# Optimization experiments

Hardware: AMD Instinct MI355X
Metric: run time of the kernel (lower is better)

The kernel has to match this reference:

```python
import jax, jax.numpy as jnp
import numpy as np

B, D, H, W, K = 32, 128, 128, 128, 32

def setup_inputs() -> dict:
    key = jax.random.key(0)
    k1, k2, k3 = jax.random.split(key, 3)
    X = jax.random.normal(k1, (B, D, H, W), dtype=jnp.float32)
    std1 = 1.0 / np.sqrt(K * D)
    codewords = jax.random.uniform(k2, (K, D), dtype=jnp.float32, minval=-std1, maxval=std1)
    scale = jax.random.uniform(k3, (K,), dtype=jnp.float32, minval=-1.0, maxval=0.0)
    return {"X": X, "codewords": codewords, "scale": scale}

def reference(X, codewords, scale):
    # X: [B, D, H, W] -> [B, N, D]
    b, d = X.shape[0], X.shape[1]
    x = X.reshape(b, d, -1).transpose(0, 2, 1)  # [B, N, D]
    x2 = jnp.sum(x * x, axis=-1, keepdims=True)            # [B, N, 1]
    c2 = jnp.sum(codewords * codewords, axis=-1)           # [K]
    xc = jnp.einsum('bnd,kd->bnk', x, codewords)           # [B, N, K]
    sl = scale * (x2 - 2.0 * xc + c2)                      # [B, N, K]
    A = jax.nn.softmax(sl, axis=2)                         # assignment weights
    # E[b,k,d] = sum_n A[b,n,k] * (x[b,n,d] - c[k,d])
    E = jnp.einsum('bnk,bnd->bkd', A, x) - jnp.sum(A, axis=1)[..., None] * codewords
    return E
```

## Files before the change

kernel.cpp:

```cpp
#include <hip/hip_runtime.h>

#define B_      32
#define D_      128
#define N_      16384
#define K_      32
#define NCHUNK  16
#define CSZ     (N_ / NCHUNK)
#define NS      512
#define NSUB    (CSZ / NS)
#define AST_STRIDE 520

#define WS_CT    0
#define WS_SC    4096
#define WS_SM2   4128
#define WS_C2S   4160
#define WS_ASUMP 4352
#define WS_EP    24576

typedef __attribute__((ext_vector_type(8))) short bf16x8;
typedef __attribute__((ext_vector_type(4))) float f32x4;

static __device__ inline unsigned short f2bf(float f) {
    unsigned int u = __float_as_uint(f);
    u += 0x7fffu + ((u >> 16) & 1u);
    return (unsigned short)(u >> 16);
}

static __device__ inline bf16x8 pack8(float4 a, float4 b) {
    bf16x8 r;
    r[0] = (short)f2bf(a.x); r[1] = (short)f2bf(a.y);
    r[2] = (short)f2bf(a.z); r[3] = (short)f2bf(a.w);
    r[4] = (short)f2bf(b.x); r[5] = (short)f2bf(b.y);
    r[6] = (short)f2bf(b.z); r[7] = (short)f2bf(b.w);
    return r;
}

__global__ void prep_kernel(const float* __restrict__ cw,
                            const float* __restrict__ scale,
                            float* __restrict__ ws) {
    const int k = blockIdx.x;
    const int l = threadIdx.x;
    float s = 0.f;
#pragma unroll
    for (int i = 0; i < 2; ++i) {
        const int d = l + i * 64;
        const float v = cw[k * D_ + d];
        s += v * v;
        ws[WS_CT + d * K_ + k] = v;
    }
#pragma unroll
    for (int o = 32; o > 0; o >>= 1) s += __shfl_down(s, o, 64);
    if (l == 0) {
        const float sc = scale[k];
        ws[WS_SC  + k] = sc;
        ws[WS_SM2 + k] = -2.f * sc;
        ws[WS_C2S + k] = sc * s;
    }
}

__global__ __launch_bounds__(512, 4) void main_kernel(
        const float* __restrict__ X,
        const float* __restrict__ ws_ro,
        float* __restrict__ AsumP,
        float* __restrict__ Ep)
{
    __shared__ __align__(16) unsigned short AsT[K_ * AST_STRIDE];

    const int t     = threadIdx.x;
    const int blk   = blockIdx.x;
    const int b     = blk >> 4;
    const int chunk = blk & 15;
    const int n0    = chunk * CSZ;

    const float* cT  = ws_ro + WS_CT;
    const float* scv = ws_ro + WS_SC;
    const float* sm2 = ws_ro + WS_SM2;
    const float* c2s = ws_ro + WS_C2S;

    const int lane = t & 63;
    const int w    = t >> 6;
    const int kh   = w & 1;
    const int dq   = w >> 1;
    const int mc   = lane & 15;
    const int q    = lane >> 4;

    const float* Xb = X + (size_t)b * ((size_t)D_ * N_);

    f32x4 accE0 = {0.f, 0.f, 0.f, 0.f};
    f32x4 accE1 = {0.f, 0.f, 0.f, 0.f};
    f32x4 accO  = {0.f, 0.f, 0.f, 0.f};

    bf16x8 ones;
#pragma unroll
    for (int i = 0; i < 8; ++i) ones[i] = (short)0x3F80;

    for (int s = 0; s < NSUB; ++s) {
        const int ns = n0 + s * NS;

        float acc[K_];
#pragma unroll
        for (int k = 0; k < K_; ++k) acc[k] = 0.f;
        float x2 = 0.f;

        const float* Xr = Xb + ns + t;
#pragma unroll 1
        for (int d0 = 0; d0 < D_; d0 += 8) {
            float xv[8];
#pragma unroll
            for (int i = 0; i < 8; ++i) xv[i] = Xr[(size_t)(d0 + i) * N_];
#pragma unroll
            for (int i = 0; i < 8; ++i) {
                x2 = fmaf(xv[i], xv[i], x2);
                const float* cr = cT + (d0 + i) * K_;
#pragma unroll
                for (int k = 0; k < K_; ++k) acc[k] = fmaf(xv[i], cr[k], acc[k]);
            }
        }

        float m = -3.4e38f;
#pragma unroll
        for (int k = 0; k < K_; ++k) {
            acc[k] = fmaf(scv[k], x2, fmaf(sm2[k], acc[k], c2s[k]));
            m = fmaxf(m, acc[k]);
        }
        float ssum = 0.f;
#pragma unroll
        for (int k = 0; k < K_; ++k) { acc[k] = __expf(acc[k] - m); ssum += acc[k]; }
        const float inv = 1.f / ssum;
#pragma unroll
        for (int k = 0; k < K_; ++k)
            AsT[k * AST_STRIDE + t] = f2bf(acc[k] * inv);

        __syncthreads();

#pragma unroll 2
        for (int ks = 0; ks < NS / 32; ++ks) {
            const int nloc = ks * 32 + q * 8;
            const bf16x8 af = *(const bf16x8*)&AsT[(kh * 16 + mc) * AST_STRIDE + nloc];

            if (dq == 0)
                accO = __builtin_amdgcn_mfma_f32_16x16x32_bf16(af, ones, accO, 0, 0, 0);

            const float* bp = Xb + (size_t)(dq * 32 + mc) * N_ + (ns + nloc);
            const float4 b0 = *(const float4*)bp;
            const float4 b1 = *(const float4*)(bp + 4);
            accE0 = __builtin_amdgcn_mfma_f32_16x16x32_bf16(af, pack8(b0, b1), accE0, 0, 0, 0);

            const float* bp2 = bp + (size_t)16 * N_;
            const float4 c0 = *(const float4*)bp2;
            const float4 c1 = *(const float4*)(bp2 + 4);
            accE1 = __builtin_amdgcn_mfma_f32_16x16x32_bf16(af, pack8(c0, c1), accE1, 0, 0, 0);
        }
        __syncthreads();
    }

    float* EpB = Ep + (size_t)blk * (K_ * D_);
#pragma unroll
    for (int r = 0; r < 4; ++r) {
        const int k = kh * 16 + q * 4 + r;
        const int d = dq * 32 + mc;
        EpB[k * D_ + d]      = accE0[r];
        EpB[k * D_ + d + 16] = accE1[r];
    }
    if (dq == 0 && mc == 0) {
#pragma unroll
        for (int r = 0; r < 4; ++r)
            AsumP[blk * K_ + kh * 16 + q * 4 + r] = accO[r];
    }
}

__global__ void finalize_kernel(const float* __restrict__ cw,
                                const float* __restrict__ AsumP,
                                const float* __restrict__ Ep,
                                float* __restrict__ out)
{
    const int idx = blockIdx.x * 256 + threadIdx.x;
    const int d = idx & 127;
    const int k = (idx >> 7) & 31;
    const int b = idx >> 12;
    float s = 0.f;
    float asum = 0.f;
#pragma unroll
    for (int c = 0; c < NCHUNK; ++c) {
        const int blk = b * NCHUNK + c;
        s    += Ep[(size_t)blk * (K_ * D_) + k * D_ + d];
        asum += AsumP[blk * K_ + k];
    }
    out[idx] = s - asum * cw[k * D_ + d];
}

extern "C" void kernel_launch(void* const* d_in, const int* in_sizes, int n_in,
                              void* d_out, int out_size, void* d_ws, size_t ws_size,
                              hipStream_t stream) {
    const float* X     = (const float*)d_in[0];
    const float* cw    = (const float*)d_in[1];
    const float* scale = (const float*)d_in[2];
    float* out = (float*)d_out;
    float* ws  = (float*)d_ws;

    float* AsumP = ws + WS_ASUMP;
    float* Ep    = ws + WS_EP;

    prep_kernel<<<K_, 64, 0, stream>>>(cw, scale, ws);
    main_kernel<<<B_ * NCHUNK, 512, 0, stream>>>(X, ws, AsumP, Ep);
    finalize_kernel<<<(B_ * K_ * D_) / 256, 256, 0, stream>>>(cw, AsumP, Ep, out);
}
```

Measured before the change: 435.1 us.

## Compute distance logits with bf16 MFMA and split N into more chunks

The scalar FP32 x·c dot product (each thread doing 32 FMAs per d) is replaced by bf16 MFMA. The codeword matrix is pre-scaled by -2*scale*log2e in the prep kernel so the softmax can use exp2f, and the max and sum reductions across lanes use shuffles. Blocks shrink to 256 threads with a 256-point subtile, and when the workspace is large enough the grid doubles to 32 chunks per batch for more parallelism. In exchange, the logits are now rounded to bf16, which may hurt accuracy, and the finalize step has more partials to sum.

After: 422.7 us. 1.03x faster.

```diff
diff --git a/kernel.cpp b/kernel.cpp
--- a/kernel.cpp
+++ b/kernel.cpp
@@ -1,38 +1,35 @@
 #include <hip/hip_runtime.h>
-
-#define B_      32
-#define D_      128
-#define N_      16384
-#define K_      32
-#define NCHUNK  16
-#define CSZ     (N_ / NCHUNK)
-#define NS      512
-#define NSUB    (CSZ / NS)
-#define AST_STRIDE 520
-
-#define WS_CT    0
-#define WS_SC    4096
-#define WS_SM2   4128
-#define WS_C2S   4160
-#define WS_ASUMP 4352
-#define WS_EP    24576
+#include <hip/hip_bf16.h>
+
+#define B_   32
+#define D_   128
+#define N_   16384
+#define K_   32
+#define NS   256
+#define AST_STRIDE 264
+
+#define WS_WBF  0
+#define WS_SC   2048
+#define WS_C2S  2080
+#define WS_EP   2112
 
 typedef __attribute__((ext_vector_type(8))) short bf16x8;
 typedef __attribute__((ext_vector_type(4))) float f32x4;
 
-static __device__ inline unsigned short f2bf(float f) {
-    unsigned int u = __float_as_uint(f);
-    u += 0x7fffu + ((u >> 16) & 1u);
-    return (unsigned short)(u >> 16);
-}
-
-static __device__ inline bf16x8 pack8(float4 a, float4 b) {
-    bf16x8 r;
-    r[0] = (short)f2bf(a.x); r[1] = (short)f2bf(a.y);
-    r[2] = (short)f2bf(a.z); r[3] = (short)f2bf(a.w);
-    r[4] = (short)f2bf(b.x); r[5] = (short)f2bf(b.y);
-    r[6] = (short)f2bf(b.z); r[7] = (short)f2bf(b.w);
+static __device__ inline unsigned int pk2(float lo, float hi) {
+    __hip_bfloat162 h = __float22bfloat162_rn(make_float2(lo, hi));
+    unsigned int r;
+    __builtin_memcpy(&r, &h, 4);
     return r;
+}
+
+static __device__ inline bf16x8 pack8(const float* v) {
+    union { unsigned int u[4]; bf16x8 f; } r;
+    r.u[0] = pk2(v[0], v[1]);
+    r.u[1] = pk2(v[2], v[3]);
+    r.u[2] = pk2(v[4], v[5]);
+    r.u[3] = pk2(v[6], v[7]);
+    return r.f;
 }
 
 __global__ void prep_kernel(const float* __restrict__ cw,
@@ -40,135 +37,181 @@
                             float* __restrict__ ws) {
     const int k = blockIdx.x;
     const int l = threadIdx.x;
+    const float sc = scale[k] * 1.44269504088896f;
+    unsigned short* Wbf = (unsigned short*)(ws + WS_WBF);
     float s = 0.f;
 #pragma unroll
     for (int i = 0; i < 2; ++i) {
         const int d = l + i * 64;
         const float v = cw[k * D_ + d];
         s += v * v;
-        ws[WS_CT + d * K_ + k] = v;
+        const float w = -2.f * sc * v;
+        unsigned int u = __float_as_uint(w);
+        u += 0x7fffu + ((u >> 16) & 1u);
+        Wbf[k * D_ + d] = (unsigned short)(u >> 16);
     }
 #pragma unroll
     for (int o = 32; o > 0; o >>= 1) s += __shfl_down(s, o, 64);
     if (l == 0) {
-        const float sc = scale[k];
         ws[WS_SC  + k] = sc;
-        ws[WS_SM2 + k] = -2.f * sc;
         ws[WS_C2S + k] = sc * s;
     }
 }
 
-__global__ __launch_bounds__(512, 4) void main_kernel(
+template<int NCHUNKT>
+__global__ __launch_bounds__(256, 4) void main_kernel(
         const float* __restrict__ X,
         const float* __restrict__ ws_ro,
         float* __restrict__ AsumP,
         float* __restrict__ Ep)
 {
+    constexpr int CSZT  = N_ / NCHUNKT;
+    constexpr int NSUBT = CSZT / NS;
+
     __shared__ __align__(16) unsigned short AsT[K_ * AST_STRIDE];
 
-    const int t     = threadIdx.x;
-    const int blk   = blockIdx.x;
-    const int b     = blk >> 4;
-    const int chunk = blk & 15;
-    const int n0    = chunk * CSZ;
-
-    const float* cT  = ws_ro + WS_CT;
-    const float* scv = ws_ro + WS_SC;
-    const float* sm2 = ws_ro + WS_SM2;
-    const float* c2s = ws_ro + WS_C2S;
-
+    const int t    = threadIdx.x;
     const int lane = t & 63;
     const int w    = t >> 6;
-    const int kh   = w & 1;
-    const int dq   = w >> 1;
     const int mc   = lane & 15;
     const int q    = lane >> 4;
 
+    const int blk   = blockIdx.x;
+    const int b     = blk / NCHUNKT;
+    const int chunk = blk % NCHUNKT;
+    const int n0    = chunk * CSZT;
+
     const float* Xb = X + (size_t)b * ((size_t)D_ * N_);
 
-    f32x4 accE0 = {0.f, 0.f, 0.f, 0.f};
-    f32x4 accE1 = {0.f, 0.f, 0.f, 0.f};
-    f32x4 accO  = {0.f, 0.f, 0.f, 0.f};
+    const unsigned short* Wbf = (const unsigned short*)(ws_ro + WS_WBF);
+    bf16x8 wf[2][4];
+#pragma unroll
+    for (int kb = 0; kb < 2; ++kb)
+#pragma unroll
+        for (int kd = 0; kd < 4; ++kd)
+            wf[kb][kd] = *(const bf16x8*)&Wbf[(kb * 16 + mc) * D_ + kd * 32 + q * 8];
+
+    float scr[2][4], c2r[2][4];
+#pragma unroll
+    for (int kb = 0; kb < 2; ++kb)
+#pragma unroll
+        for (int r = 0; r < 4; ++r) {
+            scr[kb][r] = ws_ro[WS_SC  + kb * 16 + q * 4 + r];
+            c2r[kb][r] = ws_ro[WS_C2S + kb * 16 + q * 4 + r];
+        }
 
     bf16x8 ones;
 #pragma unroll
     for (int i = 0; i < 8; ++i) ones[i] = (short)0x3F80;
 
-    for (int s = 0; s < NSUB; ++s) {
+    f32x4 accE[2][2] = {{{0.f,0.f,0.f,0.f},{0.f,0.f,0.f,0.f}},
+                        {{0.f,0.f,0.f,0.f},{0.f,0.f,0.f,0.f}}};
+    f32x4 accO[2]    = {{0.f,0.f,0.f,0.f},{0.f,0.f,0.f,0.f}};
+
+    for (int s = 0; s < NSUBT; ++s) {
         const int ns = n0 + s * NS;
 
-        float acc[K_];
-#pragma unroll
-        for (int k = 0; k < K_; ++k) acc[k] = 0.f;
-        float x2 = 0.f;
-
-        const float* Xr = Xb + ns + t;
 #pragma unroll 1
-        for (int d0 = 0; d0 < D_; d0 += 8) {
-            float xv[8];
-#pragma unroll
-            for (int i = 0; i < 8; ++i) xv[i] = Xr[(size_t)(d0 + i) * N_];
-#pragma unroll
-            for (int i = 0; i < 8; ++i) {
-                x2 = fmaf(xv[i], xv[i], x2);
-                const float* cr = cT + (d0 + i) * K_;
-#pragma unroll
-                for (int k = 0; k < K_; ++k) acc[k] = fmaf(xv[i], cr[k], acc[k]);
+        for (int cb = 0; cb < 4; ++cb) {
+            const int ntl = (w * 4 + cb) * 16;
+            const float* xp = Xb + ns + ntl + mc;
+
+            f32x4 S0 = {0.f,0.f,0.f,0.f};
+            f32x4 S1 = {0.f,0.f,0.f,0.f};
+            float x2 = 0.f;
+#pragma unroll
+            for (int kd = 0; kd < 4; ++kd) {
+                float xv[8];
+#pragma unroll
+                for (int j = 0; j < 8; ++j)
+                    xv[j] = xp[(size_t)(kd * 32 + q * 8 + j) * N_];
+#pragma unroll
+                for (int j = 0; j < 8; ++j) x2 = fmaf(xv[j], xv[j], x2);
+                const bf16x8 xb = pack8(xv);
+                S0 = __builtin_amdgcn_mfma_f32_16x16x32_bf16(wf[0][kd], xb, S0, 0, 0, 0);
+                S1 = __builtin_amdgcn_mfma_f32_16x16x32_bf16(wf[1][kd], xb, S1, 0, 0, 0);
+            }
+            x2 += __shfl_xor(x2, 16, 64);
+            x2 += __shfl_xor(x2, 32, 64);
+
+            float sl[8];
+#pragma unroll
+            for (int r = 0; r < 4; ++r) {
+                sl[r]     = fmaf(scr[0][r], x2, S0[r] + c2r[0][r]);
+                sl[4 + r] = fmaf(scr[1][r], x2, S1[r] + c2r[1][r]);
+            }
+            float m = sl[0];
+#pragma unroll
+            for (int i = 1; i < 8; ++i) m = fmaxf(m, sl[i]);
+            m = fmaxf(m, __shfl_xor(m, 16, 64));
+            m = fmaxf(m, __shfl_xor(m, 32, 64));
+            float ssum = 0.f;
+#pragma unroll
+            for (int i = 0; i < 8; ++i) { sl[i] = exp2f(sl[i] - m); ssum += sl[i]; }
+            ssum += __shfl_xor(ssum, 16, 64);
+            ssum += __shfl_xor(ssum, 32, 64);
+            const float inv = 1.f / ssum;
+
+            const int col = ntl + mc;
+#pragma unroll
+            for (int r = 0; r < 4; ++r) {
+                const unsigned int u = pk2(sl[r] * inv, sl[4 + r] * inv);
+                AsT[(q * 4 + r) * AST_STRIDE + col]        = (unsigned short)u;
+                AsT[(16 + q * 4 + r) * AST_STRIDE + col]   = (unsigned short)(u >> 16);
             }
         }
-
-        float m = -3.4e38f;
-#pragma unroll
-        for (int k = 0; k < K_; ++k) {
-            acc[k] = fmaf(scv[k], x2, fmaf(sm2[k], acc[k], c2s[k]));
-            m = fmaxf(m, acc[k]);
-        }
-        float ssum = 0.f;
-#pragma unroll
-        for (int k = 0; k < K_; ++k) { acc[k] = __expf(acc[k] - m); ssum += acc[k]; }
-        const float inv = 1.f / ssum;
-#pragma unroll
-        for (int k = 0; k < K_; ++k)
-            AsT[k * AST_STRIDE + t] = f2bf(acc[k] * inv);
-
         __syncthreads();
 
+        const int dq = w;
 #pragma unroll 2
         for (int ks = 0; ks < NS / 32; ++ks) {
-            const int nloc = ks * 32 + q * 8;
-            const bf16x8 af = *(const bf16x8*)&AsT[(kh * 16 + mc) * AST_STRIDE + nloc];
-
-            if (dq == 0)
-                accO = __builtin_amdgcn_mfma_f32_16x16x32_bf16(af, ones, accO, 0, 0, 0);
-
-            const float* bp = Xb + (size_t)(dq * 32 + mc) * N_ + (ns + nloc);
-            const float4 b0 = *(const float4*)bp;
-            const float4 b1 = *(const float4*)(bp + 4);
-            accE0 = __builtin_amdgcn_mfma_f32_16x16x32_bf16(af, pack8(b0, b1), accE0, 0, 0, 0);
-
+            const int nl = ks * 32 + q * 8;
+            const bf16x8 a0 = *(const bf16x8*)&AsT[mc * AST_STRIDE + nl];
+            const bf16x8 a1 = *(const bf16x8*)&AsT[(16 + mc) * AST_STRIDE + nl];
+
+            const float* bp = Xb + (size_t)(dq * 32 + mc) * N_ + ns + nl;
+            float xr[8];
+            *(float4*)&xr[0] = *(const float4*)bp;
+            *(float4*)&xr[4] = *(const float4*)(bp + 4);
+            const bf16x8 xb0 = pack8(xr);
             const float* bp2 = bp + (size_t)16 * N_;
-            const float4 c0 = *(const float4*)bp2;
-            const float4 c1 = *(const float4*)(bp2 + 4);
-            accE1 = __builtin_amdgcn_mfma_f32_16x16x32_bf16(af, pack8(c0, c1), accE1, 0, 0, 0);
+            *(float4*)&xr[0] = *(const float4*)bp2;
+            *(float4*)&xr[4] = *(const float4*)(bp2 + 4);
+            const bf16x8 xb1 = pack8(xr);
+
+            accE[0][0] = __builtin_amdgcn_mfma_f32_16x16x32_bf16(a0, xb0, accE[0][0], 0, 0, 0);
+            accE[0][1] = __builtin_amdgcn_mfma_f32_16x16x32_bf16(a0, xb1, accE[0][1], 0, 0, 0);
+            accE[1][0] = __builtin_amdgcn_mfma_f32_16x16x32_bf16(a1, xb0, accE[1][0], 0, 0, 0);
+            accE[1][1] = __builtin_amdgcn_mfma_f32_16x16x32_bf16(a1, xb1, accE[1][1], 0, 0, 0);
+            if (w == 0) {
+                accO[0] = __builtin_amdgcn_mfma_f32_16x16x32_bf16(a0, ones, accO[0], 0, 0, 0);
+                accO[1] = __builtin_amdgcn_mfma_f32_16x16x32_bf16(a1, ones, accO[1], 0, 0, 0);
+            }
         }
         __syncthreads();
     }
 
     float* EpB = Ep + (size_t)blk * (K_ * D_);
 #pragma unroll
-    for (int r = 0; r < 4; ++r) {
-        const int k = kh * 16 + q * 4 + r;
-        const int d = dq * 32 + mc;
-        EpB[k * D_ + d]      = accE0[r];
-        EpB[k * D_ + d + 16] = accE1[r];
-    }
-    if (dq == 0 && mc == 0) {
-#pragma unroll
-        for (int r = 0; r < 4; ++r)
-            AsumP[blk * K_ + kh * 16 + q * 4 + r] = accO[r];
-    }
-}
-
+    for (int kh = 0; kh < 2; ++kh)
+#pragma unroll
+        for (int ds = 0; ds < 2; ++ds)
+#pragma unroll
+            for (int r = 0; r < 4; ++r) {
+                const int k = kh * 16 + q * 4 + r;
+                const int d = w * 32 + ds * 16 + mc;
+                EpB[k * D_ + d] = accE[kh][ds][r];
+            }
+    if (w == 0 && mc == 0) {
+#pragma unroll
+        for (int kh = 0; kh < 2; ++kh)
+#pragma unroll
+            for (int r = 0; r < 4; ++r)
+                AsumP[blk * K_ + kh * 16 + q * 4 + r] = accO[kh][r];
+    }
+}
+
+template<int NCHUNKT>
 __global__ void finalize_kernel(const float* __restrict__ cw,
                                 const float* __restrict__ AsumP,
                                 const float* __restrict__ Ep,
@@ -178,11 +221,10 @@
     const int d = idx & 127;
     const int k = (idx >> 7) & 31;
     const int b = idx >> 12;
-    float s = 0.f;
-    float asum = 0.f;
-#pragma unroll
-    for (int c = 0; c < NCHUNK; ++c) {
-        const int blk = b * NCHUNK + c;
+    float s = 0.f, asum = 0.f;
+#pragma unroll
+    for (int c = 0; c < NCHUNKT; ++c) {
+        const int blk = b * NCHUNKT + c;
         s    += Ep[(size_t)blk * (K_ * D_) + k * D_ + d];
         asum += AsumP[blk * K_ + k];
     }
@@ -198,10 +240,18 @@
     float* out = (float*)d_out;
     float* ws  = (float*)d_ws;
 
-    float* AsumP = ws + WS_ASUMP;
-    float* Ep    = ws + WS_EP;
-
     prep_kernel<<<K_, 64, 0, stream>>>(cw, scale, ws);
-    main_kernel<<<B_ * NCHUNK, 512, 0, stream>>>(X, ws, AsumP, Ep);
-    finalize_kernel<<<(B_ * K_ * D_) / 256, 256, 0, stream>>>(cw, AsumP, Ep, out);
-}
+
+    const size_t need32 = (size_t)(WS_EP + 1024 * (K_ * D_) + 1024 * K_) * 4;
+    if (ws_size >= need32) {
+        float* Ep    = ws + WS_EP;
+        float* AsumP = Ep + (size_t)1024 * (K_ * D_);
+        main_kernel<32><<<B_ * 32, 256, 0, stream>>>(X, ws, AsumP, Ep);
+        finalize_kernel<32><<<(B_ * K_ * D_) / 256, 256, 0, stream>>>(cw, AsumP, Ep, out);
+    } else {
+        float* Ep    = ws + WS_EP;
+        float* AsumP = Ep + (size_t)512 * (K_ * D_);
+        main_kernel<16><<<B_ * 16, 256, 0, stream>>>(X, ws, AsumP, Ep);
+        finalize_kernel<16><<<(B_ * K_ * D_) / 256, 256, 0, stream>>>(cw, AsumP, Ep, out);
+    }
+}
```
